# Kernel tuning notes

Hardware: AMD Instinct MI355X
Metric: run time of the kernel (lower is better)

## Reference

```python
import jax, jax.numpy as jnp
import numpy as np

E, D, H, T = 8, 1024, 4096, 8192  # num_expert, d_model, d_hidden, total_tokens


def setup_inputs() -> dict:
    key = jax.random.key(0)
    k1, k2, k3, k4, k5 = jax.random.split(key, 5)
    inp = jax.random.normal(k1, (T, D), dtype=jnp.float32)
    # FMoELinear weights: [E, out_features, in_features], bias [E, out_features]
    w1 = jax.random.normal(k2, (E, H, D), dtype=jnp.float32) * 0.02
    b1 = jax.random.normal(k3, (E, H), dtype=jnp.float32) * 0.02
    w2 = jax.random.normal(k4, (E, D, H), dtype=jnp.float32) * 0.02
    b2 = jax.random.normal(k5, (E, D), dtype=jnp.float32) * 0.02
    # tokens are contiguous per expert; equal split here (counts may vary in general)
    fwd_expert_count = jnp.full((E,), T // E, dtype=jnp.int32)
    return {"inp": inp, "w1": w1, "b1": b1, "w2": w2, "b2": b2,
            "fwd_expert_count": fwd_expert_count}


def _expert_ids(counts, n_tokens):
    # token t belongs to expert e iff cumsum(counts)[e-1] <= t < cumsum(counts)[e]
    offsets = jnp.cumsum(counts)  # [E]
    t = jnp.arange(n_tokens)
    return jnp.sum(t[:, None] >= offsets[None, :], axis=1)  # [T] in [0, E]


def _grouped_linear(x, W, b, eid):
    # grouped GEMM: y[t] = W[eid[t]] @ x[t] + b[eid[t]]; tokens with eid >= E -> 0
    n_exp = W.shape[0]
    acc = jnp.zeros((x.shape[0], W.shape[1]), dtype=x.dtype)
    for e in range(n_exp):  # small fixed loop over experts
        ye = x @ W[e].T + b[e]
        acc = acc + jnp.where((eid == e)[:, None], ye, jnp.zeros((), x.dtype))
    return acc


def reference(inp, w1, b1, w2, b2, fwd_expert_count):
    eid = _expert_ids(fwd_expert_count, inp.shape[0])
    h = _grouped_linear(inp, w1, b1, eid)   # [T, H]
    h = jax.nn.gelu(h)
    out = _grouped_linear(h, w2, b2, eid)   # [T, D]
    return out
```

## Files before the change

kernel.cpp:

```cpp
#include <hip/hip_runtime.h>
#include <hip/hip_bf16.h>
#include <cstdint>
#include <cstddef>


using bf16 = __hip_bfloat16;
typedef __attribute__((ext_vector_type(8))) short bf16x8;
typedef __attribute__((ext_vector_type(4))) float f32x4;

#define BM 128
#define BN 128
#define BK 32

typedef const __attribute__((address_space(1))) unsigned int g_u32;
typedef __attribute__((address_space(3))) unsigned int l_u32;

__device__ __forceinline__ void async16(void* lds, const void* g) {
  __builtin_amdgcn_global_load_lds((g_u32*)g, (l_u32*)lds, 16, 0, 0);
}

__device__ __forceinline__ float gelu_f(float x) {
  const float c0 = 0.7978845608028654f;
  const float c1 = 0.044715f;
  float u = c0 * (x + c1 * x * x * x);
  float t = 1.0f - 2.0f / (__expf(2.0f * u) + 1.0f);
  return 0.5f * x * (1.0f + t);
}

__global__ __launch_bounds__(256) void f32_to_bf16(
    const float* __restrict__ in, bf16* __restrict__ out, size_t n) {
  size_t i = ((size_t)blockIdx.x * blockDim.x + threadIdx.x) * 8;
  const size_t stride = (size_t)gridDim.x * blockDim.x * 8;
  for (; i < n; i += stride) {
    f32x4 lo = *(const f32x4*)(in + i);
    f32x4 hi = *(const f32x4*)(in + i + 4);
    bf16 cv[8];
#pragma unroll
    for (int k = 0; k < 4; ++k) {
      cv[k]     = __float2bfloat16(lo[k]);
      cv[k + 4] = __float2bfloat16(hi[k]);
    }
    *(bf16x8*)(out + i) = *(const bf16x8*)cv;
  }
}

__global__ __launch_bounds__(256) void gemm_bt_bf16(
    const bf16* __restrict__ A,
    const bf16* __restrict__ B,
    const float* __restrict__ bias,
    void* __restrict__ Cv,
    const int* __restrict__ counts,
    int E, int N, int K, int c_is_bf16_gelu)
{
  __shared__ alignas(16) bf16 As[BM * BK];
  __shared__ alignas(16) bf16 Bs[BN * BK];

  const int tid  = threadIdx.x;
  const int lane = tid & 63;
  const int wave = tid >> 6;
  const int m0 = blockIdx.y * BM;
  const int n0 = blockIdx.x * BN;

  int eid = 0;
  {
    long long cum = 0;
    for (int e = 0; e < E; ++e) { cum += counts[e]; if (m0 >= cum) eid = e + 1; }
  }

  const int wrow = (wave >> 1) * 64;
  const int wcol = (wave & 1) * 64;

  f32x4 acc[4][4] = {};

  if (eid < E) {
    const bf16* Bexp = B + (size_t)eid * (size_t)N * (size_t)K;

    const int rA = lane >> 2;
    const int sA = (lane & 3) * 8;

    const int frow = lane & 15;
    const int fk   = (lane >> 4) * 8;

    for (int kt = 0; kt < K; kt += BK) {
#pragma unroll
      for (int c = 0; c < 2; ++c) {
        const int chunk = wave * 2 + c;
        const int row = chunk * 16 + rA;
        async16(&As[chunk * 16 * BK],
                A + (size_t)(m0 + row) * K + kt + sA);
        async16(&Bs[chunk * 16 * BK],
                Bexp + (size_t)(n0 + row) * K + kt + sA);
      }
      __syncthreads();

      bf16x8 af[4], bfr[4];
#pragma unroll
      for (int i = 0; i < 4; ++i)
        af[i] = *(const bf16x8*)&As[(wrow + i * 16 + frow) * BK + fk];
#pragma unroll
      for (int j = 0; j < 4; ++j)
        bfr[j] = *(const bf16x8*)&Bs[(wcol + j * 16 + frow) * BK + fk];

#pragma unroll
      for (int i = 0; i < 4; ++i)
#pragma unroll
        for (int j = 0; j < 4; ++j)
          acc[i][j] = __builtin_amdgcn_mfma_f32_16x16x32_bf16(af[i], bfr[j], acc[i][j], 0, 0, 0);

      __syncthreads();
    }
  }

  const int crow = (lane >> 4) * 4;
  const int ccol = lane & 15;
  const int do_gelu = c_is_bf16_gelu;

  if (eid < E) {
    float bv[4];
#pragma unroll
    for (int j = 0; j < 4; ++j)
      bv[j] = bias[(size_t)eid * N + n0 + wcol + j * 16 + ccol];
#pragma unroll
    for (int i = 0; i < 4; ++i) {
#pragma unroll
      for (int r = 0; r < 4; ++r) {
        size_t grow = (size_t)(m0 + wrow + i * 16 + crow + r);
#pragma unroll
        for (int j = 0; j < 4; ++j) {
          float v = acc[i][j][r] + bv[j];
          size_t idx = grow * N + n0 + wcol + j * 16 + ccol;
          if (do_gelu) ((bf16*)Cv)[idx] = __float2bfloat16(gelu_f(v));
          else         ((float*)Cv)[idx] = v;
        }
      }
    }
  } else {
#pragma unroll
    for (int i = 0; i < 4; ++i) {
#pragma unroll
      for (int r = 0; r < 4; ++r) {
        size_t grow = (size_t)(m0 + wrow + i * 16 + crow + r);
#pragma unroll
        for (int j = 0; j < 4; ++j) {
          size_t idx = grow * N + n0 + wcol + j * 16 + ccol;
          if (do_gelu) ((bf16*)Cv)[idx] = __float2bfloat16(0.0f);
          else         ((float*)Cv)[idx] = 0.0f;
        }
      }
    }
  }
}

__device__ __forceinline__ void stage_f32(const float* g, bf16* lds,
                                          int srow, int seg, int ldg) {
#pragma unroll
  for (int h = 0; h < 2; ++h) {
    const float* p = g + (size_t)(srow + h * 64) * ldg + seg;
    f32x4 lo = *(const f32x4*)(p);
    f32x4 hi = *(const f32x4*)(p + 4);
    bf16 cv[8];
#pragma unroll
    for (int i = 0; i < 4; ++i) {
      cv[i]     = __float2bfloat16(lo[i]);
      cv[i + 4] = __float2bfloat16(hi[i]);
    }
    *(bf16x8*)&lds[(srow + h * 64) * BK + seg] = *(const bf16x8*)cv;
  }
}

__device__ __forceinline__ void stage_bf16(const bf16* g, bf16* lds,
                                           int srow, int seg, int ldg) {
#pragma unroll
  for (int h = 0; h < 2; ++h) {
    const bf16* p = g + (size_t)(srow + h * 64) * ldg + seg;
    *(bf16x8*)&lds[(srow + h * 64) * BK + seg] = *(const bf16x8*)p;
  }
}

template <bool AF32>
__global__ __launch_bounds__(256) void grouped_gemm_bt(
    const void* __restrict__ Av, const float* __restrict__ B,
    const float* __restrict__ bias, void* __restrict__ Cv,
    const int* __restrict__ counts, int E, int N, int K, int c_is_bf16_gelu)
{
  __shared__ alignas(16) bf16 As[BM * BK];
  __shared__ alignas(16) bf16 Bs[BN * BK];

  const int tid  = threadIdx.x;
  const int lane = tid & 63;
  const int wave = tid >> 6;
  const int m0 = blockIdx.y * BM;
  const int n0 = blockIdx.x * BN;

  int eid = 0;
  {
    long long cum = 0;
    for (int e = 0; e < E; ++e) { cum += counts[e]; if (m0 >= cum) eid = e + 1; }
  }

  const int wrow = (wave >> 1) * 64;
  const int wcol = (wave & 1) * 64;

  f32x4 acc[4][4] = {};

  if (eid < E) {
    const float* Bexp = B + (size_t)eid * (size_t)N * (size_t)K;
    const int srow = tid >> 2;
    const int seg  = (tid & 3) * 8;
    const int frow = lane & 15;
    const int fk   = (lane >> 4) * 8;

    for (int kt = 0; kt < K; kt += BK) {
      if (AF32)
        stage_f32((const float*)Av + (size_t)(m0 + srow) * K + kt - (size_t)srow * K,
                  As, srow, seg, K);
      else
        stage_bf16((const bf16*)Av + (size_t)(m0 + srow) * K + kt - (size_t)srow * K,
                   As, srow, seg, K);
      stage_f32(Bexp + (size_t)(n0 + srow) * K + kt - (size_t)srow * K,
                Bs, srow, seg, K);
      __syncthreads();

      bf16x8 af[4], bfr[4];
#pragma unroll
      for (int i = 0; i < 4; ++i)
        af[i] = *(const bf16x8*)&As[(wrow + i * 16 + frow) * BK + fk];
#pragma unroll
      for (int j = 0; j < 4; ++j)
        bfr[j] = *(const bf16x8*)&Bs[(wcol + j * 16 + frow) * BK + fk];

#pragma unroll
      for (int i = 0; i < 4; ++i)
#pragma unroll
        for (int j = 0; j < 4; ++j)
          acc[i][j] = __builtin_amdgcn_mfma_f32_16x16x32_bf16(af[i], bfr[j], acc[i][j], 0, 0, 0);

      __syncthreads();
    }
  }

  const int crow = (lane >> 4) * 4;
  const int ccol = lane & 15;
  const int do_gelu = c_is_bf16_gelu;

  if (eid < E) {
    float bv[4];
#pragma unroll
    for (int j = 0; j < 4; ++j)
      bv[j] = bias[(size_t)eid * N + n0 + wcol + j * 16 + ccol];
#pragma unroll
    for (int i = 0; i < 4; ++i) {
#pragma unroll
      for (int r = 0; r < 4; ++r) {
        size_t grow = (size_t)(m0 + wrow + i * 16 + crow + r);
#pragma unroll
        for (int j = 0; j < 4; ++j) {
          float v = acc[i][j][r] + bv[j];
          size_t idx = grow * N + n0 + wcol + j * 16 + ccol;
          if (do_gelu) ((bf16*)Cv)[idx] = __float2bfloat16(gelu_f(v));
          else         ((float*)Cv)[idx] = v;
        }
      }
    }
  } else {
#pragma unroll
    for (int i = 0; i < 4; ++i) {
#pragma unroll
      for (int r = 0; r < 4; ++r) {
        size_t grow = (size_t)(m0 + wrow + i * 16 + crow + r);
#pragma unroll
        for (int j = 0; j < 4; ++j) {
          size_t idx = grow * N + n0 + wcol + j * 16 + ccol;
          if (do_gelu) ((bf16*)Cv)[idx] = __float2bfloat16(0.0f);
          else         ((float*)Cv)[idx] = 0.0f;
        }
      }
    }
  }
}

extern "C" void kernel_launch(void* const* d_in, const int* in_sizes, int n_in,
                              void* d_out, int out_size, void* d_ws, size_t ws_size,
                              hipStream_t stream) {
  const float* inp = (const float*)d_in[0];
  const float* w1  = (const float*)d_in[1];
  const float* b1  = (const float*)d_in[2];
  const float* w2  = (const float*)d_in[3];
  const float* b2  = (const float*)d_in[4];
  const int* cnt   = (const int*)d_in[5];
  float* out = (float*)d_out;

  const int E = in_sizes[5];
  const int H = in_sizes[2] / E;
  const int D = in_sizes[4] / E;
  const int T = in_sizes[0] / D;

  const size_t szH = (size_t)T * H * sizeof(bf16);
  const size_t szX = (size_t)T * D * sizeof(bf16);
  const size_t szW = (size_t)E * (size_t)H * D * sizeof(bf16);

  dim3 blk(256);

  if (ws_size >= szH + szX + szW) {
    bf16* h  = (bf16*)d_ws;
    bf16* xb = (bf16*)((char*)d_ws + szH);
    bf16* wb = (bf16*)((char*)d_ws + szH + szX);

    const size_t nX = (size_t)T * D;
    const size_t nW = (size_t)E * (size_t)H * D;

    f32_to_bf16<<<dim3(1024), blk, 0, stream>>>(inp, xb, nX);
    f32_to_bf16<<<dim3(2048), blk, 0, stream>>>(w1, wb, nW);
    gemm_bt_bf16<<<dim3(H / BN, T / BM), blk, 0, stream>>>(xb, wb, b1, h, cnt, E, H, D, 1);
    f32_to_bf16<<<dim3(2048), blk, 0, stream>>>(w2, wb, nW);
    gemm_bt_bf16<<<dim3(D / BN, T / BM), blk, 0, stream>>>(h, wb, b2, out, cnt, E, D, H, 0);
  } else {
    bf16* h = (bf16*)d_ws;
    grouped_gemm_bt<true><<<dim3(H / BN, T / BM), blk, 0, stream>>>(inp, w1, b1, h, cnt, E, H, D, 1);
    grouped_gemm_bt<false><<<dim3(D / BN, T / BM), blk, 0, stream>>>(h, w2, b2, out, cnt, E, D, H, 0);
  }
}
```

Measured before the change: 553.5 us.

## Fuse fp32-to-bf16 weight conversion into GEMM B-tile loads

Drops the two separate weight conversion passes (each reading 128MB of fp32 and writing bf16) and has the grouped GEMM load fp32 weight tiles directly into LDS through an XOR-swizzled layout, converting to bf16 in registers before the MFMA. This removes the conversion kernels' memory traffic and launches. In exchange each GEMM block reads twice as many bytes per B tile, uses double the B LDS footprint, and adds conversion ALU work in the inner loop. Because M tiles are 64 per expert, weights are re-read many times.

```diff
diff --git a/kernel.cpp b/kernel.cpp
--- a/kernel.cpp
+++ b/kernel.cpp
@@ -44,16 +44,16 @@
   }
 }
 
-__global__ __launch_bounds__(256) void gemm_bt_bf16(
+__global__ __launch_bounds__(256) void gemm_bt_a16_b32(
     const bf16* __restrict__ A,
-    const bf16* __restrict__ B,
+    const float* __restrict__ B,
     const float* __restrict__ bias,
     void* __restrict__ Cv,
     const int* __restrict__ counts,
     int E, int N, int K, int c_is_bf16_gelu)
 {
-  __shared__ alignas(16) bf16 As[BM * BK];
-  __shared__ alignas(16) bf16 Bs[BN * BK];
+  __shared__ alignas(16) bf16  As[BM * BK];
+  __shared__ alignas(16) float BsF[BN * BK];
 
   const int tid  = threadIdx.x;
   const int lane = tid & 63;
@@ -73,13 +73,17 @@
   f32x4 acc[4][4] = {};
 
   if (eid < E) {
-    const bf16* Bexp = B + (size_t)eid * (size_t)N * (size_t)K;
+    const float* Bexp = B + (size_t)eid * (size_t)N * (size_t)K;
 
     const int rA = lane >> 2;
     const int sA = (lane & 3) * 8;
 
+    const int rB   = lane >> 3;
+    const int colB = 4 * ((lane & 7) ^ (rB & 7));
+
     const int frow = lane & 15;
     const int fk   = (lane >> 4) * 8;
+    const int fkb  = fk * 4;
 
     for (int kt = 0; kt < K; kt += BK) {
 #pragma unroll
@@ -88,8 +92,13 @@
         const int row = chunk * 16 + rA;
         async16(&As[chunk * 16 * BK],
                 A + (size_t)(m0 + row) * K + kt + sA);
-        async16(&Bs[chunk * 16 * BK],
-                Bexp + (size_t)(n0 + row) * K + kt + sA);
+      }
+#pragma unroll
+      for (int c = 0; c < 4; ++c) {
+        const int chunk = wave * 4 + c;
+        const int row = chunk * 8 + rB;
+        async16(&BsF[chunk * 256],
+                Bexp + (size_t)(n0 + row) * K + kt + colB);
       }
       __syncthreads();
 
@@ -98,8 +107,20 @@
       for (int i = 0; i < 4; ++i)
         af[i] = *(const bf16x8*)&As[(wrow + i * 16 + frow) * BK + fk];
 #pragma unroll
-      for (int j = 0; j < 4; ++j)
-        bfr[j] = *(const bf16x8*)&Bs[(wcol + j * 16 + frow) * BK + fk];
+      for (int j = 0; j < 4; ++j) {
+        const int brow = wcol + j * 16 + frow;
+        uintptr_t a1 = (uintptr_t)BsF + (uintptr_t)brow * 128
+                     + (uintptr_t)(fkb ^ ((brow & 7) << 4));
+        f32x4 lo = *(const f32x4*)a1;
+        f32x4 hi = *(const f32x4*)(a1 ^ 16);
+        bf16 cv[8];
+#pragma unroll
+        for (int q = 0; q < 4; ++q) {
+          cv[q]     = __float2bfloat16(lo[q]);
+          cv[q + 4] = __float2bfloat16(hi[q]);
+        }
+        bfr[j] = *(const bf16x8*)cv;
+      }
 
 #pragma unroll
       for (int i = 0; i < 4; ++i)
@@ -297,23 +318,18 @@
 
   const size_t szH = (size_t)T * H * sizeof(bf16);
   const size_t szX = (size_t)T * D * sizeof(bf16);
-  const size_t szW = (size_t)E * (size_t)H * D * sizeof(bf16);
 
   dim3 blk(256);
 
-  if (ws_size >= szH + szX + szW) {
+  if (ws_size >= szH + szX) {
     bf16* h  = (bf16*)d_ws;
     bf16* xb = (bf16*)((char*)d_ws + szH);
-    bf16* wb = (bf16*)((char*)d_ws + szH + szX);
-
-    const size_t nX = (size_t)T * D;
-    const size_t nW = (size_t)E * (size_t)H * D;
-
-    f32_to_bf16<<<dim3(1024), blk, 0, stream>>>(inp, xb, nX);
-    f32_to_bf16<<<dim3(2048), blk, 0, stream>>>(w1, wb, nW);
-    gemm_bt_bf16<<<dim3(H / BN, T / BM), blk, 0, stream>>>(xb, wb, b1, h, cnt, E, H, D, 1);
-    f32_to_bf16<<<dim3(2048), blk, 0, stream>>>(w2, wb, nW);
-    gemm_bt_bf16<<<dim3(D / BN, T / BM), blk, 0, stream>>>(h, wb, b2, out, cnt, E, D, H, 0);
+
+    f32_to_bf16<<<dim3(1024), blk, 0, stream>>>(inp, xb, (size_t)T * D);
+    gemm_bt_a16_b32<<<dim3(H / BN, T / BM), blk, 0, stream>>>(
+        xb, w1, b1, h, cnt, E, H, D, 1);
+    gemm_bt_a16_b32<<<dim3(D / BN, T / BM), blk, 0, stream>>>(
+        h, w2, b2, out, cnt, E, D, H, 0);
   } else {
     bf16* h = (bf16*)d_ws;
     grouped_gemm_bt<true><<<dim3(H / BN, T / BM), blk, 0, stream>>>(inp, w1, b1, h, cnt, E, H, D, 1);
```

Measured after the change: 621.4 us. 12.3% more time.

## Double-buffer LDS tiles, remap workgroups across XCDs, fuse conversion kernels

Applied to the files above, without the earlier changes.

The bf16 GEMM now double-buffers its A/B LDS tiles, prefetching the next K-tile with async global-to-LDS loads while the current tile feeds the MFMAs, using explicit vmcnt waits and barriers. Workgroup IDs are remapped so consecutive tiles land on the same XCD, improving L2 reuse of weights and activations. The input and w1 fp32-to-bf16 conversions are merged into one launch to cut launch overhead. This doubles LDS per block, which may reduce occupancy, and the hand-written vmcnt counting must match the number of outstanding loads.

```diff
diff --git a/kernel.cpp b/kernel.cpp
--- a/kernel.cpp
+++ b/kernel.cpp
@@ -27,21 +27,61 @@
   return 0.5f * x * (1.0f + t);
 }
 
-__global__ __launch_bounds__(256) void f32_to_bf16(
-    const float* __restrict__ in, bf16* __restrict__ out, size_t n) {
-  size_t i = ((size_t)blockIdx.x * blockDim.x + threadIdx.x) * 8;
+__global__ __launch_bounds__(256) void f32_to_bf16_2(
+    const float* __restrict__ a, bf16* __restrict__ oa, size_t na,
+    const float* __restrict__ b, bf16* __restrict__ ob, size_t nb) {
   const size_t stride = (size_t)gridDim.x * blockDim.x * 8;
-  for (; i < n; i += stride) {
-    f32x4 lo = *(const f32x4*)(in + i);
-    f32x4 hi = *(const f32x4*)(in + i + 4);
+  const size_t base = ((size_t)blockIdx.x * blockDim.x + threadIdx.x) * 8;
+  for (size_t i = base; i < na; i += stride) {
+    f32x4 lo = *(const f32x4*)(a + i);
+    f32x4 hi = *(const f32x4*)(a + i + 4);
     bf16 cv[8];
 #pragma unroll
     for (int k = 0; k < 4; ++k) {
       cv[k]     = __float2bfloat16(lo[k]);
       cv[k + 4] = __float2bfloat16(hi[k]);
     }
-    *(bf16x8*)(out + i) = *(const bf16x8*)cv;
-  }
+    *(bf16x8*)(oa + i) = *(const bf16x8*)cv;
+  }
+  for (size_t i = base; i < nb; i += stride) {
+    f32x4 lo = *(const f32x4*)(b + i);
+    f32x4 hi = *(const f32x4*)(b + i + 4);
+    bf16 cv[8];
+#pragma unroll
+    for (int k = 0; k < 4; ++k) {
+      cv[k]     = __float2bfloat16(lo[k]);
+      cv[k + 4] = __float2bfloat16(hi[k]);
+    }
+    *(bf16x8*)(ob + i) = *(const bf16x8*)cv;
+  }
+}
+
+__device__ __forceinline__ void stage_tile(bf16* AsBuf, bf16* BsBuf,
+    const bf16* __restrict__ A, const bf16* __restrict__ Bexp,
+    int m0, int n0, int kt, int K, int wave, int rA, int sA) {
+#pragma unroll
+  for (int c = 0; c < 2; ++c) {
+    const int chunk = wave * 2 + c;
+    const int row = chunk * 16 + rA;
+    async16(&AsBuf[chunk * 16 * BK], A    + (size_t)(m0 + row) * K + kt + sA);
+    async16(&BsBuf[chunk * 16 * BK], Bexp + (size_t)(n0 + row) * K + kt + sA);
+  }
+}
+
+__device__ __forceinline__ void mma_tile(const bf16* As, const bf16* Bs,
+    int wrow, int wcol, int frow, int fk, f32x4 (&acc)[4][4]) {
+  bf16x8 af[4], bfr[4];
+#pragma unroll
+  for (int i = 0; i < 4; ++i)
+    af[i] = *(const bf16x8*)&As[(wrow + i * 16 + frow) * BK + fk];
+#pragma unroll
+  for (int j = 0; j < 4; ++j)
+    bfr[j] = *(const bf16x8*)&Bs[(wcol + j * 16 + frow) * BK + fk];
+#pragma unroll
+  for (int i = 0; i < 4; ++i)
+#pragma unroll
+    for (int j = 0; j < 4; ++j)
+      acc[i][j] = __builtin_amdgcn_mfma_f32_16x16x32_bf16(af[i], bfr[j], acc[i][j], 0, 0, 0);
 }
 
 __global__ __launch_bounds__(256) void gemm_bt_bf16(
@@ -52,14 +92,21 @@
     const int* __restrict__ counts,
     int E, int N, int K, int c_is_bf16_gelu)
 {
-  __shared__ alignas(16) bf16 As[BM * BK];
-  __shared__ alignas(16) bf16 Bs[BN * BK];
+  __shared__ alignas(16) bf16 As[2][BM * BK];
+  __shared__ alignas(16) bf16 Bs[2][BN * BK];
 
   const int tid  = threadIdx.x;
   const int lane = tid & 63;
   const int wave = tid >> 6;
-  const int m0 = blockIdx.y * BM;
-  const int n0 = blockIdx.x * BN;
+
+  const int gx   = gridDim.x;
+  const int nwg  = gx * gridDim.y;
+  const int orig = blockIdx.y * gx + blockIdx.x;
+  const int qq = nwg >> 3, rr = nwg & 7;
+  const int xcd = orig & 7, lo = orig >> 3;
+  const int wgid = (xcd < rr ? xcd * (qq + 1) : rr * (qq + 1) + (xcd - rr) * qq) + lo;
+  const int m0 = (wgid / gx) * BM;
+  const int n0 = (wgid % gx) * BN;
 
   int eid = 0;
   {
@@ -74,41 +121,27 @@
 
   if (eid < E) {
     const bf16* Bexp = B + (size_t)eid * (size_t)N * (size_t)K;
-
     const int rA = lane >> 2;
     const int sA = (lane & 3) * 8;
-
     const int frow = lane & 15;
     const int fk   = (lane >> 4) * 8;
-
-    for (int kt = 0; kt < K; kt += BK) {
-#pragma unroll
-      for (int c = 0; c < 2; ++c) {
-        const int chunk = wave * 2 + c;
-        const int row = chunk * 16 + rA;
-        async16(&As[chunk * 16 * BK],
-                A + (size_t)(m0 + row) * K + kt + sA);
-        async16(&Bs[chunk * 16 * BK],
-                Bexp + (size_t)(n0 + row) * K + kt + sA);
-      }
-      __syncthreads();
-
-      bf16x8 af[4], bfr[4];
-#pragma unroll
-      for (int i = 0; i < 4; ++i)
-        af[i] = *(const bf16x8*)&As[(wrow + i * 16 + frow) * BK + fk];
-#pragma unroll
-      for (int j = 0; j < 4; ++j)
-        bfr[j] = *(const bf16x8*)&Bs[(wcol + j * 16 + frow) * BK + fk];
-
-#pragma unroll
-      for (int i = 0; i < 4; ++i)
-#pragma unroll
-        for (int j = 0; j < 4; ++j)
-          acc[i][j] = __builtin_amdgcn_mfma_f32_16x16x32_bf16(af[i], bfr[j], acc[i][j], 0, 0, 0);
-
-      __syncthreads();
-    }
+    const int nt = K / BK;
+
+    stage_tile(As[0], Bs[0], A, Bexp, m0, n0, 0, K, wave, rA, sA);
+
+    int cur = 0;
+    for (int t = 0; t < nt - 1; ++t) {
+      stage_tile(As[cur ^ 1], Bs[cur ^ 1], A, Bexp, m0, n0, (t + 1) * BK,
+                 K, wave, rA, sA);
+      asm volatile("s_waitcnt vmcnt(4)" ::: "memory");
+      __builtin_amdgcn_s_barrier();
+      mma_tile(As[cur], Bs[cur], wrow, wcol, frow, fk, acc);
+      __builtin_amdgcn_s_barrier();
+      cur ^= 1;
+    }
+    asm volatile("s_waitcnt vmcnt(0)" ::: "memory");
+    __builtin_amdgcn_s_barrier();
+    mma_tile(As[cur], Bs[cur], wrow, wcol, frow, fk, acc);
   }
 
   const int crow = (lane >> 4) * 4;
@@ -168,8 +201,8 @@
   }
 }
 
-__device__ __forceinline__ void stage_bf16(const bf16* g, bf16* lds,
-                                           int srow, int seg, int ldg) {
+__device__ __forceinline__ void stage_bf16f(const bf16* g, bf16* lds,
+                                            int srow, int seg, int ldg) {
 #pragma unroll
   for (int h = 0; h < 2; ++h) {
     const bf16* p = g + (size_t)(srow + h * 64) * ldg + seg;
@@ -215,8 +248,8 @@
         stage_f32((const float*)Av + (size_t)(m0 + srow) * K + kt - (size_t)srow * K,
                   As, srow, seg, K);
       else
-        stage_bf16((const bf16*)Av + (size_t)(m0 + srow) * K + kt - (size_t)srow * K,
-                   As, srow, seg, K);
+        stage_bf16f((const bf16*)Av + (size_t)(m0 + srow) * K + kt - (size_t)srow * K,
+                    As, srow, seg, K);
       stage_f32(Bexp + (size_t)(n0 + srow) * K + kt - (size_t)srow * K,
                 Bs, srow, seg, K);
       __syncthreads();
@@ -309,11 +342,12 @@
     const size_t nX = (size_t)T * D;
     const size_t nW = (size_t)E * (size_t)H * D;
 
-    f32_to_bf16<<<dim3(1024), blk, 0, stream>>>(inp, xb, nX);
-    f32_to_bf16<<<dim3(2048), blk, 0, stream>>>(w1, wb, nW);
-    gemm_bt_bf16<<<dim3(H / BN, T / BM), blk, 0, stream>>>(xb, wb, b1, h, cnt, E, H, D, 1);
-    f32_to_bf16<<<dim3(2048), blk, 0, stream>>>(w2, wb, nW);
-    gemm_bt_bf16<<<dim3(D / BN, T / BM), blk, 0, stream>>>(h, wb, b2, out, cnt, E, D, H, 0);
+    f32_to_bf16_2<<<dim3(2048), blk, 0, stream>>>(inp, xb, nX, w1, wb, nW);
+    gemm_bt_bf16<<<dim3(H / BN, T / BM), blk, 0, stream>>>(
+        xb, wb, b1, h, cnt, E, H, D, 1);
+    f32_to_bf16_2<<<dim3(2048), blk, 0, stream>>>(w2, wb, nW, nullptr, nullptr, 0);
+    gemm_bt_bf16<<<dim3(D / BN, T / BM), blk, 0, stream>>>(
+        h, wb, b2, out, cnt, E, D, H, 0);
   } else {
     bf16* h = (bf16*)d_ws;
     grouped_gemm_bt<true><<<dim3(H / BN, T / BM), blk, 0, stream>>>(inp, w1, b1, h, cnt, E, H, D, 1);
```

New measurement: 558.5 us. About the same (+0.9%).

## Triple-buffer bf16 grouped GEMM with larger tiles, LDS swizzle and XCD remap

Applied to the files above, without the earlier changes.

The bf16 grouped GEMM moves to 256x128x64 tiles on 512 threads, with a three-stage async global-to-LDS pipeline driven by explicit vmcnt waits and a single barrier per k-step. Loads use an XOR swizzle to reduce LDS bank conflicts, and workgroup IDs are remapped so neighbouring tiles land on the same XCD for L2 reuse. The conversions of x, w1 and w2 are fused into one launch when the workspace can hold both converted weight sets. The cost is more LDS and a larger workspace, and the hand-written waitcnt logic is fragile if the compiler reorders loads.

```diff
diff --git a/kernel.cpp b/kernel.cpp
--- a/kernel.cpp
+++ b/kernel.cpp
@@ -8,9 +8,9 @@
 typedef __attribute__((ext_vector_type(8))) short bf16x8;
 typedef __attribute__((ext_vector_type(4))) float f32x4;
 
-#define BM 128
+#define BM 256
 #define BN 128
-#define BK 32
+#define BK 64
 
 typedef const __attribute__((address_space(1))) unsigned int g_u32;
 typedef __attribute__((address_space(3))) unsigned int l_u32;
@@ -27,24 +27,39 @@
   return 0.5f * x * (1.0f + t);
 }
 
-__global__ __launch_bounds__(256) void f32_to_bf16(
-    const float* __restrict__ in, bf16* __restrict__ out, size_t n) {
-  size_t i = ((size_t)blockIdx.x * blockDim.x + threadIdx.x) * 8;
+__device__ __forceinline__ void cvt8(const float* in, bf16* out, size_t i) {
+  f32x4 lo = *(const f32x4*)(in + i);
+  f32x4 hi = *(const f32x4*)(in + i + 4);
+  bf16 cv[8];
+#pragma unroll
+  for (int k = 0; k < 4; ++k) {
+    cv[k]     = __float2bfloat16(lo[k]);
+    cv[k + 4] = __float2bfloat16(hi[k]);
+  }
+  *(bf16x8*)(out + i) = *(const bf16x8*)cv;
+}
+
+__global__ __launch_bounds__(256) void f32_to_bf16_2(
+    const float* __restrict__ a, bf16* __restrict__ oa, size_t na,
+    const float* __restrict__ b, bf16* __restrict__ ob, size_t nb) {
   const size_t stride = (size_t)gridDim.x * blockDim.x * 8;
-  for (; i < n; i += stride) {
-    f32x4 lo = *(const f32x4*)(in + i);
-    f32x4 hi = *(const f32x4*)(in + i + 4);
-    bf16 cv[8];
-#pragma unroll
-    for (int k = 0; k < 4; ++k) {
-      cv[k]     = __float2bfloat16(lo[k]);
-      cv[k + 4] = __float2bfloat16(hi[k]);
-    }
-    *(bf16x8*)(out + i) = *(const bf16x8*)cv;
-  }
-}
-
-__global__ __launch_bounds__(256) void gemm_bt_bf16(
+  const size_t base = ((size_t)blockIdx.x * blockDim.x + threadIdx.x) * 8;
+  for (size_t i = base; i < na; i += stride) cvt8(a, oa, i);
+  for (size_t i = base; i < nb; i += stride) cvt8(b, ob, i);
+}
+
+__global__ __launch_bounds__(256) void f32_to_bf16_3(
+    const float* __restrict__ a, bf16* __restrict__ oa, size_t na,
+    const float* __restrict__ b, bf16* __restrict__ ob, size_t nb,
+    const float* __restrict__ c, bf16* __restrict__ oc, size_t nc) {
+  const size_t stride = (size_t)gridDim.x * blockDim.x * 8;
+  const size_t base = ((size_t)blockIdx.x * blockDim.x + threadIdx.x) * 8;
+  for (size_t i = base; i < na; i += stride) cvt8(a, oa, i);
+  for (size_t i = base; i < nb; i += stride) cvt8(b, ob, i);
+  for (size_t i = base; i < nc; i += stride) cvt8(c, oc, i);
+}
+
+__global__ __launch_bounds__(512) void gemm_bt_bf16(
     const bf16* __restrict__ A,
     const bf16* __restrict__ B,
     const float* __restrict__ bias,
@@ -52,14 +67,21 @@
     const int* __restrict__ counts,
     int E, int N, int K, int c_is_bf16_gelu)
 {
-  __shared__ alignas(16) bf16 As[BM * BK];
-  __shared__ alignas(16) bf16 Bs[BN * BK];
+  __shared__ alignas(16) bf16 As[3][BM * BK];
+  __shared__ alignas(16) bf16 Bs[3][BN * BK];
 
   const int tid  = threadIdx.x;
   const int lane = tid & 63;
   const int wave = tid >> 6;
-  const int m0 = blockIdx.y * BM;
-  const int n0 = blockIdx.x * BN;
+
+  const int gx   = gridDim.x;
+  const int nwg  = gx * gridDim.y;
+  const int orig = blockIdx.y * gx + blockIdx.x;
+  const int qq = nwg >> 3, rr = nwg & 7;
+  const int xcd = orig & 7, lo = orig >> 3;
+  const int wgid = (xcd < rr ? xcd * (qq + 1) : rr * (qq + 1) + (xcd - rr) * qq) + lo;
+  const int m0 = (wgid / gx) * BM;
+  const int n0 = (wgid % gx) * BN;
 
   int eid = 0;
   {
@@ -67,47 +89,64 @@
     for (int e = 0; e < E; ++e) { cum += counts[e]; if (m0 >= cum) eid = e + 1; }
   }
 
-  const int wrow = (wave >> 1) * 64;
-  const int wcol = (wave & 1) * 64;
+  const int wm = wave >> 1;
+  const int wn = wave & 1;
 
   f32x4 acc[4][4] = {};
 
   if (eid < E) {
-    const bf16* Bexp = B + (size_t)eid * (size_t)N * (size_t)K;
-
-    const int rA = lane >> 2;
-    const int sA = (lane & 3) * 8;
-
-    const int frow = lane & 15;
-    const int fk   = (lane >> 4) * 8;
-
-    for (int kt = 0; kt < K; kt += BK) {
-#pragma unroll
-      for (int c = 0; c < 2; ++c) {
-        const int chunk = wave * 2 + c;
-        const int row = chunk * 16 + rA;
-        async16(&As[chunk * 16 * BK],
-                A + (size_t)(m0 + row) * K + kt + sA);
-        async16(&Bs[chunk * 16 * BK],
-                Bexp + (size_t)(n0 + row) * K + kt + sA);
-      }
-      __syncthreads();
-
-      bf16x8 af[4], bfr[4];
-#pragma unroll
-      for (int i = 0; i < 4; ++i)
-        af[i] = *(const bf16x8*)&As[(wrow + i * 16 + frow) * BK + fk];
-#pragma unroll
-      for (int j = 0; j < 4; ++j)
-        bfr[j] = *(const bf16x8*)&Bs[(wcol + j * 16 + frow) * BK + fk];
-
-#pragma unroll
-      for (int i = 0; i < 4; ++i)
+    const bf16* Ag = A + (size_t)m0 * K;
+    const bf16* Bg = B + (size_t)eid * (size_t)N * (size_t)K + (size_t)n0 * K;
+
+    const int rlane = wave * 8 + (lane >> 3);
+    const int swz   = ((lane & 7) ^ ((lane >> 3) & 7)) * 8;
+
+    const int abase = (wm * 64 + (lane & 15)) * BK;
+    const int bbase = (wn * 64 + (lane & 15)) * BK;
+    const int swzf0 = (((lane >> 4) + 0) ^ (lane & 7)) * 8;
+    const int swzf1 = (((lane >> 4) + 4) ^ (lane & 7)) * 8;
+
+    const int nt = K / BK;
+
+    auto STAGE = [&](int bi, int kt) {
+#pragma unroll
+      for (int c = 0; c < 4; ++c)
+        async16(&As[bi][c * 4096 + wave * 512],
+                Ag + (size_t)(c * 64 + rlane) * K + kt + swz);
+#pragma unroll
+      for (int c = 0; c < 2; ++c)
+        async16(&Bs[bi][c * 4096 + wave * 512],
+                Bg + (size_t)(c * 64 + rlane) * K + kt + swz);
+    };
+
+    auto MMA = [&](const bf16* Ab, const bf16* Bb) {
+#pragma unroll
+      for (int ks = 0; ks < 2; ++ks) {
+        const int sw = ks ? swzf1 : swzf0;
+        bf16x8 a[4], b[4];
+#pragma unroll
+        for (int i = 0; i < 4; ++i)
+          a[i] = *(const bf16x8*)&Ab[abase + i * 16 * BK + sw];
 #pragma unroll
         for (int j = 0; j < 4; ++j)
-          acc[i][j] = __builtin_amdgcn_mfma_f32_16x16x32_bf16(af[i], bfr[j], acc[i][j], 0, 0, 0);
-
-      __syncthreads();
+          b[j] = *(const bf16x8*)&Bb[bbase + j * 16 * BK + sw];
+#pragma unroll
+        for (int i = 0; i < 4; ++i)
+#pragma unroll
+          for (int j = 0; j < 4; ++j)
+            acc[i][j] = __builtin_amdgcn_mfma_f32_16x16x32_bf16(a[i], b[j], acc[i][j], 0, 0, 0);
+      }
+    };
+
+    STAGE(0, 0);
+    STAGE(1, BK);
+
+    for (int t = 0; t < nt; ++t) {
+      if (t < nt - 1) asm volatile("s_waitcnt vmcnt(6)" ::: "memory");
+      else            asm volatile("s_waitcnt vmcnt(0)" ::: "memory");
+      __builtin_amdgcn_s_barrier();
+      if (t + 2 < nt) STAGE((t + 2) % 3, (t + 2) * BK);
+      MMA(As[t % 3], Bs[t % 3]);
     }
   }
 
@@ -119,16 +158,16 @@
     float bv[4];
 #pragma unroll
     for (int j = 0; j < 4; ++j)
-      bv[j] = bias[(size_t)eid * N + n0 + wcol + j * 16 + ccol];
+      bv[j] = bias[(size_t)eid * N + n0 + wn * 64 + j * 16 + ccol];
 #pragma unroll
     for (int i = 0; i < 4; ++i) {
 #pragma unroll
       for (int r = 0; r < 4; ++r) {
-        size_t grow = (size_t)(m0 + wrow + i * 16 + crow + r);
+        size_t grow = (size_t)(m0 + wm * 64 + i * 16 + crow + r);
 #pragma unroll
         for (int j = 0; j < 4; ++j) {
           float v = acc[i][j][r] + bv[j];
-          size_t idx = grow * N + n0 + wcol + j * 16 + ccol;
+          size_t idx = grow * N + n0 + wn * 64 + j * 16 + ccol;
           if (do_gelu) ((bf16*)Cv)[idx] = __float2bfloat16(gelu_f(v));
           else         ((float*)Cv)[idx] = v;
         }
@@ -139,10 +178,10 @@
     for (int i = 0; i < 4; ++i) {
 #pragma unroll
       for (int r = 0; r < 4; ++r) {
-        size_t grow = (size_t)(m0 + wrow + i * 16 + crow + r);
+        size_t grow = (size_t)(m0 + wm * 64 + i * 16 + crow + r);
 #pragma unroll
         for (int j = 0; j < 4; ++j) {
-          size_t idx = grow * N + n0 + wcol + j * 16 + ccol;
+          size_t idx = grow * N + n0 + wn * 64 + j * 16 + ccol;
           if (do_gelu) ((bf16*)Cv)[idx] = __float2bfloat16(0.0f);
           else         ((float*)Cv)[idx] = 0.0f;
         }
@@ -150,6 +189,9 @@
     }
   }
 }
+
+#define FBM 128
+#define FBK 32
 
 __device__ __forceinline__ void stage_f32(const float* g, bf16* lds,
                                           int srow, int seg, int ldg) {
@@ -164,16 +206,16 @@
       cv[i]     = __float2bfloat16(lo[i]);
       cv[i + 4] = __float2bfloat16(hi[i]);
     }
-    *(bf16x8*)&lds[(srow + h * 64) * BK + seg] = *(const bf16x8*)cv;
-  }
-}
-
-__device__ __forceinline__ void stage_bf16(const bf16* g, bf16* lds,
-                                           int srow, int seg, int ldg) {
+    *(bf16x8*)&lds[(srow + h * 64) * FBK + seg] = *(const bf16x8*)cv;
+  }
+}
+
+__device__ __forceinline__ void stage_bf16f(const bf16* g, bf16* lds,
+                                            int srow, int seg, int ldg) {
 #pragma unroll
   for (int h = 0; h < 2; ++h) {
     const bf16* p = g + (size_t)(srow + h * 64) * ldg + seg;
-    *(bf16x8*)&lds[(srow + h * 64) * BK + seg] = *(const bf16x8*)p;
+    *(bf16x8*)&lds[(srow + h * 64) * FBK + seg] = *(const bf16x8*)p;
   }
 }
 
@@ -183,14 +225,14 @@
     const float* __restrict__ bias, void* __restrict__ Cv,
     const int* __restrict__ counts, int E, int N, int K, int c_is_bf16_gelu)
 {
-  __shared__ alignas(16) bf16 As[BM * BK];
-  __shared__ alignas(16) bf16 Bs[BN * BK];
+  __shared__ alignas(16) bf16 As[FBM * FBK];
+  __shared__ alignas(16) bf16 Bs[FBM * FBK];
 
   const int tid  = threadIdx.x;
   const int lane = tid & 63;
   const int wave = tid >> 6;
-  const int m0 = blockIdx.y * BM;
-  const int n0 = blockIdx.x * BN;
+  const int m0 = blockIdx.y * FBM;
+  const int n0 = blockIdx.x * FBM;
 
   int eid = 0;
   {
@@ -210,13 +252,13 @@
     const int frow = lane & 15;
     const int fk   = (lane >> 4) * 8;
 
-    for (int kt = 0; kt < K; kt += BK) {
+    for (int kt = 0; kt < K; kt += FBK) {
       if (AF32)
         stage_f32((const float*)Av + (size_t)(m0 + srow) * K + kt - (size_t)srow * K,
                   As, srow, seg, K);
       else
-        stage_bf16((const bf16*)Av + (size_t)(m0 + srow) * K + kt - (size_t)srow * K,
-                   As, srow, seg, K);
+        stage_bf16f((const bf16*)Av + (size_t)(m0 + srow) * K + kt - (size_t)srow * K,
+                    As, srow, seg, K);
       stage_f32(Bexp + (size_t)(n0 + srow) * K + kt - (size_t)srow * K,
                 Bs, srow, seg, K);
       __syncthreads();
@@ -224,10 +266,10 @@
       bf16x8 af[4], bfr[4];
 #pragma unroll
       for (int i = 0; i < 4; ++i)
-        af[i] = *(const bf16x8*)&As[(wrow + i * 16 + frow) * BK + fk];
+        af[i] = *(const bf16x8*)&As[(wrow + i * 16 + frow) * FBK + fk];
 #pragma unroll
       for (int j = 0; j < 4; ++j)
-        bfr[j] = *(const bf16x8*)&Bs[(wcol + j * 16 + frow) * BK + fk];
+        bfr[j] = *(const bf16x8*)&Bs[(wcol + j * 16 + frow) * FBK + fk];
 
 #pragma unroll
       for (int i = 0; i < 4; ++i)
@@ -299,24 +341,37 @@
   const size_t szX = (size_t)T * D * sizeof(bf16);
   const size_t szW = (size_t)E * (size_t)H * D * sizeof(bf16);
 
-  dim3 blk(256);
-
-  if (ws_size >= szH + szX + szW) {
+  const size_t nX = (size_t)T * D;
+  const size_t nW = (size_t)E * (size_t)H * D;
+
+  dim3 cblk(256), gblk(512);
+  dim3 g1(H / BN, T / BM);
+  dim3 g2(D / BN, T / BM);
+
+  if (ws_size >= szH + szX + 2 * szW) {
+    bf16* h   = (bf16*)d_ws;
+    bf16* xb  = (bf16*)((char*)d_ws + szH);
+    bf16* w1b = (bf16*)((char*)d_ws + szH + szX);
+    bf16* w2b = (bf16*)((char*)d_ws + szH + szX + szW);
+
+    f32_to_bf16_3<<<dim3(4096), cblk, 0, stream>>>(inp, xb, nX, w1, w1b, nW,
+                                                   w2, w2b, nW);
+    gemm_bt_bf16<<<g1, gblk, 0, stream>>>(xb, w1b, b1, h, cnt, E, H, D, 1);
+    gemm_bt_bf16<<<g2, gblk, 0, stream>>>(h, w2b, b2, out, cnt, E, D, H, 0);
+  } else if (ws_size >= szH + szX + szW) {
     bf16* h  = (bf16*)d_ws;
     bf16* xb = (bf16*)((char*)d_ws + szH);
     bf16* wb = (bf16*)((char*)d_ws + szH + szX);
 
-    const size_t nX = (size_t)T * D;
-    const size_t nW = (size_t)E * (size_t)H * D;
-
-    f32_to_bf16<<<dim3(1024), blk, 0, stream>>>(inp, xb, nX);
-    f32_to_bf16<<<dim3(2048), blk, 0, stream>>>(w1, wb, nW);
-    gemm_bt_bf16<<<dim3(H / BN, T / BM), blk, 0, stream>>>(xb, wb, b1, h, cnt, E, H, D, 1);
-    f32_to_bf16<<<dim3(2048), blk, 0, stream>>>(w2, wb, nW);
-    gemm_bt_bf16<<<dim3(D / BN, T / BM), blk, 0, stream>>>(h, wb, b2, out, cnt, E, D, H, 0);
+    f32_to_bf16_2<<<dim3(2048), cblk, 0, stream>>>(inp, xb, nX, w1, wb, nW);
+    gemm_bt_bf16<<<g1, gblk, 0, stream>>>(xb, wb, b1, h, cnt, E, H, D, 1);
+    f32_to_bf16_2<<<dim3(2048), cblk, 0, stream>>>(w2, wb, nW, nullptr, nullptr, 0);
+    gemm_bt_bf16<<<g2, gblk, 0, stream>>>(h, wb, b2, out, cnt, E, D, H, 0);
   } else {
     bf16* h = (bf16*)d_ws;
-    grouped_gemm_bt<true><<<dim3(H / BN, T / BM), blk, 0, stream>>>(inp, w1, b1, h, cnt, E, H, D, 1);
-    grouped_gemm_bt<false><<<dim3(D / BN, T / BM), blk, 0, stream>>>(h, w2, b2, out, cnt, E, D, H, 0);
-  }
-}
+    grouped_gemm_bt<true><<<dim3(H / FBM, T / FBM), cblk, 0, stream>>>(
+        inp, w1, b1, h, cnt, E, H, D, 1);
+    grouped_gemm_bt<false><<<dim3(D / FBM, T / FBM), cblk, 0, stream>>>(
+        h, w2, b2, out, cnt, E, D, H, 0);
+  }
+}
```

New measurement: 578.8 us. 1.05x slower.
